# Optimization experiments

Hardware: AMD Instinct MI355X
Metric: run time of the kernel (lower is better)

## Reference

```python
import jax, jax.numpy as jnp
import numpy as np

NUM_NODES = 100000
EMBED_DIM = 128
HIDDEN = 128
NUM_EDGES = 1600000


def gcn_conv(x, W, b, src, dst, num_nodes):
    """PyG GCNConv: x' = D^{-1/2} (A+I) D^{-1/2} (x W) + b, symmetric norm with self-loops."""
    x = x @ W  # [N, out]
    loops = jnp.arange(num_nodes, dtype=src.dtype)
    s = jnp.concatenate([src, loops])  # sources incl. self-loops
    d = jnp.concatenate([dst, loops])  # targets incl. self-loops
    deg = jax.ops.segment_sum(jnp.ones_like(d, dtype=x.dtype), d, num_segments=num_nodes)
    dis = jnp.where(deg > 0, jax.lax.rsqrt(deg), 0.0)  # deg^{-1/2}, 0 where isolated
    norm = dis[s] * dis[d]  # [E+N]
    msg = x[s] * norm[:, None]  # gather + scale
    out = jax.ops.segment_sum(msg, d, num_segments=num_nodes)  # scatter-add
    return out + b


def setup_inputs() -> dict:
    key = jax.random.key(0)
    k1, k2, k3, k4, k5, k6 = jax.random.split(key, 6)
    edge_index = jax.random.randint(k1, (2, NUM_EDGES), 0, NUM_NODES, dtype=jnp.int64)
    edge_attr = jax.random.normal(k2, (NUM_EDGES,), dtype=jnp.float32)
    emb = jax.random.normal(k3, (NUM_NODES, EMBED_DIM), dtype=jnp.float32) * 0.1
    W1 = jax.random.normal(k4, (EMBED_DIM, HIDDEN), dtype=jnp.float32) * (1.0 / np.sqrt(EMBED_DIM))
    b1 = jnp.zeros((HIDDEN,), dtype=jnp.float32)
    W2 = jax.random.normal(k5, (HIDDEN, HIDDEN), dtype=jnp.float32) * (1.0 / np.sqrt(HIDDEN))
    b2 = jnp.zeros((HIDDEN,), dtype=jnp.float32)
    return {"edge_index": edge_index, "edge_attr": edge_attr, "emb": emb,
            "W1": W1, "b1": b1, "W2": W2, "b2": b2}


def reference(edge_index, edge_attr, emb, W1, b1, W2, b2):
    src, dst = edge_index[0], edge_index[1]
    x = gcn_conv(emb, W1, b1, src, dst, NUM_NODES)
    x = jax.nn.relu(x)
    x = gcn_conv(x, W2, b2, src, dst, NUM_NODES)
    return x
```

## Files before the change

### kernel.cpp

```cpp
#include <hip/hip_runtime.h>

#define EMB 128
#define NBUC 1024
#define NPART 256

typedef __attribute__((ext_vector_type(8))) short short8;
typedef __attribute__((ext_vector_type(4))) float f32x4;

__device__ __forceinline__ unsigned short f2bf(float f) {
    union { float f; unsigned int i; } v; v.f = f;
    unsigned int x = v.i;
    x += 0x7fffu + ((x >> 16) & 1u);
    return (unsigned short)(x >> 16);
}
__device__ __forceinline__ void acc_bf4(uint2 v, float& a0, float& a1, float& a2, float& a3) {
    union { unsigned int i; float f; } t;
    t.i = v.x << 16;          a0 += t.f;
    t.i = v.x & 0xffff0000u;  a1 += t.f;
    t.i = v.y << 16;          a2 += t.f;
    t.i = v.y & 0xffff0000u;  a3 += t.f;
}


__global__ __launch_bounds__(256) void p1_hist(const int* __restrict__ dst,
                                               int* __restrict__ BH, int E, int chunk) {
    __shared__ int h[NBUC];
    for (int i = threadIdx.x; i < NBUC; i += 256) h[i] = 0;
    __syncthreads();
    int s = blockIdx.x * chunk;
    int e = min(E, s + chunk);
    for (int i = s + threadIdx.x; i < e; i += 256)
        atomicAdd(&h[dst[i] >> 7], 1);
    __syncthreads();
    for (int i = threadIdx.x; i < NBUC; i += 256)
        BH[blockIdx.x * NBUC + i] = h[i];
}

__global__ __launch_bounds__(256) void p_tot(const int* __restrict__ BH,
                                             int* __restrict__ tot) {
    int b = blockIdx.x * 256 + threadIdx.x;
    int s = 0;
    for (int blk = 0; blk < NPART; ++blk) s += BH[blk * NBUC + b];
    tot[b] = s;
}

__global__ __launch_bounds__(1024) void p_scan(const int* __restrict__ tot,
                                               int* __restrict__ base, int E) {
    __shared__ int a[NBUC];
    int t = threadIdx.x;
    int v0 = tot[t];
    a[t] = v0;
    __syncthreads();
    for (int off = 1; off < NBUC; off <<= 1) {
        int v = (t >= off) ? a[t - off] : 0;
        __syncthreads();
        a[t] += v;
        __syncthreads();
    }
    base[t] = a[t] - v0;
    if (t == NBUC - 1) base[NBUC] = E;
}

__global__ __launch_bounds__(256) void p_offs(int* __restrict__ BH,
                                              const int* __restrict__ base) {
    int b = blockIdx.x * 256 + threadIdx.x;
    int run = base[b];
    for (int blk = 0; blk < NPART; ++blk) {
        int* p = &BH[blk * NBUC + b];
        int v = *p;
        *p = run;
        run += v;
    }
}

__global__ __launch_bounds__(256) void p2_scatter(const int* __restrict__ src,
                                                  const int* __restrict__ dst,
                                                  const int* __restrict__ BH,
                                                  int* __restrict__ part,
                                                  int E, int chunk) {
    __shared__ int cnt[NBUC];
    for (int i = threadIdx.x; i < NBUC; i += 256)
        cnt[i] = BH[blockIdx.x * NBUC + i];
    __syncthreads();
    int s = blockIdx.x * chunk;
    int e = min(E, s + chunk);
    for (int i = s + threadIdx.x; i < e; i += 256) {
        int d = dst[i];
        int pos = atomicAdd(&cnt[d >> 7], 1);
        part[pos] = src[i] | ((d & 127) << 17);
    }
}

__global__ __launch_bounds__(256) void p3_csr(const int* __restrict__ part,
                                              const int* __restrict__ base,
                                              int* __restrict__ R, int* __restrict__ adj,
                                              float* __restrict__ dis, int N, int E) {
    __shared__ int hist[128];
    __shared__ int sc[128];
    __shared__ int cnt[128];
    int b = blockIdx.x;
    int n0 = b * 128;
    int nn = min(128, N - n0);
    int s = base[b], e = base[b + 1];
    int t = threadIdx.x;

    if (t < 128) hist[t] = 0;
    __syncthreads();
    for (int i = s + t; i < e; i += 256)
        atomicAdd(&hist[part[i] >> 17], 1);
    __syncthreads();

    if (t < 128) sc[t] = hist[t];
    __syncthreads();
    for (int off = 1; off < 128; off <<= 1) {
        int v = 0;
        if (t < 128 && t >= off) v = sc[t - off];
        __syncthreads();
        if (t < 128) sc[t] += v;
        __syncthreads();
    }
    if (t < 128) {
        int excl = sc[t] - hist[t];
        cnt[t] = excl;
        if (t < nn) {
            R[n0 + t] = s + excl;
            dis[n0 + t] = rsqrtf((float)hist[t] + 1.0f);
        }
    }
    if (b == 0 && t == 0) R[N] = E;
    __syncthreads();

    for (int i = s + t; i < e; i += 256) {
        int p = part[i];
        int pos = atomicAdd(&cnt[p >> 17], 1);
        adj[s + pos] = p & 0x1FFFF;
    }
}

__global__ __launch_bounds__(256) void k_prep_w(const float* __restrict__ W,
                                                unsigned short* __restrict__ Ws) {
    int idx = blockIdx.x * 256 + threadIdx.x;
    int k = idx >> 7, n = idx & 127;
    int kk = k >> 5, q = (k >> 3) & 3, j = k & 7;
    int ct = n >> 4, nn = n & 15;
    int didx = ((((kk * 8 + ct) * 4 + q) * 16 + nn) << 3) + j;
    Ws[didx] = f2bf(W[idx]);
}

template <bool XBF16>
__global__ __launch_bounds__(256) void k_gemm_mfma(
    const void* Xv, const unsigned short* __restrict__ Wsw,
    const float* __restrict__ dis, unsigned short* Y, int N)
{
    __shared__ __align__(16) unsigned short lds[16384];

    {
        const uint4* srcp = (const uint4*)Wsw;
        uint4* dstp = (uint4*)lds;
        for (int i = threadIdx.x; i < 2048; i += 256) dstp[i] = srcp[i];
    }
    __syncthreads();

    const int wave = threadIdx.x >> 6;
    const int lane = threadIdx.x & 63;
    const int q = lane >> 4, nn = lane & 15;
    const int row0 = blockIdx.x * 64 + wave * 16;
    const int arow = row0 + nn;
    const int arc = arow < N ? arow : N - 1;

    f32x4 acc[8];
#pragma unroll
    for (int ct = 0; ct < 8; ++ct) acc[ct] = (f32x4){0.f, 0.f, 0.f, 0.f};

#pragma unroll
    for (int kk = 0; kk < 4; ++kk) {
        short8 af;
        if (XBF16) {
            af = *(const short8*)((const unsigned short*)Xv + (size_t)arc * EMB + kk * 32 + q * 8);
        } else {
            const float* xp = (const float*)Xv + (size_t)arc * EMB + kk * 32 + q * 8;
            float4 u0 = *(const float4*)xp;
            float4 u1 = *(const float4*)(xp + 4);
            af[0] = (short)f2bf(u0.x); af[1] = (short)f2bf(u0.y);
            af[2] = (short)f2bf(u0.z); af[3] = (short)f2bf(u0.w);
            af[4] = (short)f2bf(u1.x); af[5] = (short)f2bf(u1.y);
            af[6] = (short)f2bf(u1.z); af[7] = (short)f2bf(u1.w);
        }
#pragma unroll
        for (int ct = 0; ct < 8; ++ct) {
            short8 bf = ((const short8*)lds)[(kk * 8 + ct) * 64 + lane];
            acc[ct] = __builtin_amdgcn_mfma_f32_16x16x32_bf16(af, bf, acc[ct], 0, 0, 0);
        }
    }

    __syncthreads();

    float dv[4];
#pragma unroll
    for (int r = 0; r < 4; ++r) {
        int gm = row0 + q * 4 + r;
        dv[r] = dis[gm < N ? gm : N - 1];
    }
#pragma unroll
    for (int ct = 0; ct < 8; ++ct) {
#pragma unroll
        for (int r = 0; r < 4; ++r) {
            int ml = wave * 16 + q * 4 + r;
            lds[ml * 136 + ct * 16 + nn] = f2bf(acc[ct][r] * dv[r]);
        }
    }
    __syncthreads();

    const int rbase = blockIdx.x * 64;
    for (int i = threadIdx.x; i < 1024; i += 256) {
        int row = i >> 4, off = i & 15;
        int grow = rbase + row;
        if (grow < N) {
            uint4 v = *(const uint4*)(lds + row * 136 + off * 8);
            *((uint4*)(Y + (size_t)grow * EMB) + off) = v;
        }
    }
}

template <bool RELU, bool BF16OUT>
__global__ __launch_bounds__(256) void k_gather_finalize(
    const int* __restrict__ R, const int* __restrict__ adj,
    const unsigned short* __restrict__ Y, const float* __restrict__ dis,
    const float* __restrict__ bias, void* __restrict__ Outv, int N)
{
    int t = blockIdx.x * 256 + threadIdx.x;
    int n = t >> 5;
    if (n >= N) return;
    int j = (t & 31) * 4;

    int rs = R[n], re = R[n + 1];

    float a0 = 0.f, a1 = 0.f, a2 = 0.f, a3 = 0.f;
    uint2 sv = *(const uint2*)(Y + (size_t)n * EMB + j);
    acc_bf4(sv, a0, a1, a2, a3);

    int e = rs;
    for (; e + 3 < re; e += 4) {
        int s0 = adj[e], s1 = adj[e + 1], s2 = adj[e + 2], s3 = adj[e + 3];
        uint2 v0 = *(const uint2*)(Y + (size_t)s0 * EMB + j);
        uint2 v1 = *(const uint2*)(Y + (size_t)s1 * EMB + j);
        uint2 v2 = *(const uint2*)(Y + (size_t)s2 * EMB + j);
        uint2 v3 = *(const uint2*)(Y + (size_t)s3 * EMB + j);
        acc_bf4(v0, a0, a1, a2, a3);
        acc_bf4(v1, a0, a1, a2, a3);
        acc_bf4(v2, a0, a1, a2, a3);
        acc_bf4(v3, a0, a1, a2, a3);
    }
    for (; e < re; ++e) {
        uint2 v0 = *(const uint2*)(Y + (size_t)adj[e] * EMB + j);
        acc_bf4(v0, a0, a1, a2, a3);
    }

    float dv = dis[n];
    float4 b = *(const float4*)(bias + j);
    float o0 = dv * a0 + b.x;
    float o1 = dv * a1 + b.y;
    float o2 = dv * a2 + b.z;
    float o3 = dv * a3 + b.w;
    if (RELU) {
        o0 = fmaxf(o0, 0.f); o1 = fmaxf(o1, 0.f);
        o2 = fmaxf(o2, 0.f); o3 = fmaxf(o3, 0.f);
    }
    if (BF16OUT) {
        ushort4 o = { f2bf(o0), f2bf(o1), f2bf(o2), f2bf(o3) };
        *(ushort4*)((unsigned short*)Outv + (size_t)n * EMB + j) = o;
    } else {
        float4 o = { o0, o1, o2, o3 };
        *(float4*)((float*)Outv + (size_t)n * EMB + j) = o;
    }
}

extern "C" void kernel_launch(void* const* d_in, const int* in_sizes, int n_in,
                              void* d_out, int out_size, void* d_ws, size_t ws_size,
                              hipStream_t stream) {
    const int* ei = (const int*)d_in[0];
    const int E = in_sizes[0] / 2;
    const float* emb = (const float*)d_in[2];
    const int N = in_sizes[2] / EMB;
    const float* W1 = (const float*)d_in[3];
    const float* b1 = (const float*)d_in[4];
    const float* W2 = (const float*)d_in[5];
    const float* b2 = (const float*)d_in[6];
    float* out = (float*)d_out;

    const int* src = ei;
    const int* dstp = ei + E;

    char* w = (char*)d_ws;
    auto take = [&](size_t bytes) { char* p = w; w += (bytes + 511) & ~(size_t)511; return p; };
    float* dis  = (float*)take((size_t)N * 4);
    int*   R    = (int*)  take((size_t)(N + 1) * 4);
    int*   base = (int*)  take((size_t)(NBUC + 1) * 4);
    int*   tot  = (int*)  take((size_t)NBUC * 4);
    int*   adj  = (int*)  take((size_t)E * 4);
    unsigned short* W1s = (unsigned short*)take((size_t)EMB * EMB * 2);
    unsigned short* W2s = (unsigned short*)take((size_t)EMB * EMB * 2);
    unsigned short* Hb  = (unsigned short*)take((size_t)N * EMB * 2);
    int*   part = (int*)Hb;
    int*   BH   = (int*)((char*)Hb + (((size_t)E * 4 + 511) & ~(size_t)511));
    unsigned short* Y1b = (unsigned short*)d_out;

    const int NB = (N + 127) / 128;
    const int chunk = (E + NPART - 1) / NPART;
    const int gM = (N + 63) / 64;
    const int gG = (N * 32 + 255) / 256;

    p1_hist   <<<NPART, 256, 0, stream>>>(dstp, BH, E, chunk);
    p_tot     <<<NBUC / 256, 256, 0, stream>>>(BH, tot);
    p_scan    <<<1, NBUC, 0, stream>>>(tot, base, E);
    p_offs    <<<NBUC / 256, 256, 0, stream>>>(BH, base);
    p2_scatter<<<NPART, 256, 0, stream>>>(src, dstp, BH, part, E, chunk);
    p3_csr    <<<NB, 256, 0, stream>>>(part, base, R, adj, dis, N, E);

    k_prep_w<<<64, 256, 0, stream>>>(W1, W1s);
    k_prep_w<<<64, 256, 0, stream>>>(W2, W2s);

    k_gemm_mfma<false><<<gM, 256, 0, stream>>>(emb, W1s, dis, Y1b, N);
    k_gather_finalize<true, true><<<gG, 256, 0, stream>>>(R, adj, Y1b, dis, b1, Hb, N);

    k_gemm_mfma<true><<<gM, 256, 0, stream>>>(Hb, W2s, dis, Hb, N);
    k_gather_finalize<false, false><<<gG, 256, 0, stream>>>(R, adj, Hb, dis, b2, out, N);
}
```

Baseline: 343.8 us.

## Store bf16 activations slot-blocked so each XCD gathers one L2-resident feature slice

Rewrites the GEMM output and gather input into a feature-sliced layout: eight 16-column slots, each stored contiguously over all nodes. The gather kernel assigns slot = blockIdx & 7. Because blocks are dispatched round-robin across the 8 XCDs, each XCD then works on a single ~3.2MB slice, which can stay in its own L2 instead of spilling random gathers to HBM or Infinity Cache. The cost is that each edge index is now read eight times, and each neighbour access is a 32-byte read per lane pair rather than part of a 256-byte row read.

```diff
diff --git a/kernel.cpp b/kernel.cpp
--- a/kernel.cpp
+++ b/kernel.cpp
@@ -3,6 +3,7 @@
 #define EMB 128
 #define NBUC 1024
 #define NPART 256
+#define NSLOT 8
 
 typedef __attribute__((ext_vector_type(8))) short short8;
 typedef __attribute__((ext_vector_type(4))) float f32x4;
@@ -13,12 +14,16 @@
     x += 0x7fffu + ((x >> 16) & 1u);
     return (unsigned short)(x >> 16);
 }
-__device__ __forceinline__ void acc_bf4(uint2 v, float& a0, float& a1, float& a2, float& a3) {
+__device__ __forceinline__ void acc_bf8(uint4 v, float a[8]) {
     union { unsigned int i; float f; } t;
-    t.i = v.x << 16;          a0 += t.f;
-    t.i = v.x & 0xffff0000u;  a1 += t.f;
-    t.i = v.y << 16;          a2 += t.f;
-    t.i = v.y & 0xffff0000u;  a3 += t.f;
+    t.i = v.x << 16;          a[0] += t.f;
+    t.i = v.x & 0xffff0000u;  a[1] += t.f;
+    t.i = v.y << 16;          a[2] += t.f;
+    t.i = v.y & 0xffff0000u;  a[3] += t.f;
+    t.i = v.z << 16;          a[4] += t.f;
+    t.i = v.z & 0xffff0000u;  a[5] += t.f;
+    t.i = v.w << 16;          a[6] += t.f;
+    t.i = v.w & 0xffff0000u;  a[7] += t.f;
 }
 
 
@@ -176,7 +181,10 @@
     for (int kk = 0; kk < 4; ++kk) {
         short8 af;
         if (XBF16) {
-            af = *(const short8*)((const unsigned short*)Xv + (size_t)arc * EMB + kk * 32 + q * 8);
+            const int slot = kk * 2 + (q >> 1);
+            const int off = (q & 1) * 8;
+            af = *(const short8*)((const unsigned short*)Xv +
+                                  ((size_t)slot * N + arc) * 16 + off);
         } else {
             const float* xp = (const float*)Xv + (size_t)arc * EMB + kk * 32 + q * 8;
             float4 u0 = *(const float4*)xp;
@@ -213,65 +221,76 @@
 
     const int rbase = blockIdx.x * 64;
     for (int i = threadIdx.x; i < 1024; i += 256) {
-        int row = i >> 4, off = i & 15;
-        int grow = rbase + row;
+        int slot = i >> 7, r2 = (i >> 1) & 63, off = (i & 1) * 8;
+        int grow = rbase + r2;
         if (grow < N) {
-            uint4 v = *(const uint4*)(lds + row * 136 + off * 8);
-            *((uint4*)(Y + (size_t)grow * EMB) + off) = v;
+            uint4 v = *(const uint4*)(lds + r2 * 136 + slot * 16 + off);
+            *(uint4*)(Y + ((size_t)slot * N + grow) * 16 + off) = v;
         }
     }
 }
 
 template <bool RELU, bool BF16OUT>
-__global__ __launch_bounds__(256) void k_gather_finalize(
+__global__ __launch_bounds__(256) void k_gather_blocked(
     const int* __restrict__ R, const int* __restrict__ adj,
-    const unsigned short* __restrict__ Y, const float* __restrict__ dis,
+    const unsigned short* __restrict__ Yb, const float* __restrict__ dis,
     const float* __restrict__ bias, void* __restrict__ Outv, int N)
 {
-    int t = blockIdx.x * 256 + threadIdx.x;
-    int n = t >> 5;
+    const int slot = blockIdx.x & 7;
+    const int n = (blockIdx.x >> 3) * 128 + (threadIdx.x >> 1);
+    const int h = threadIdx.x & 1;
     if (n >= N) return;
-    int j = (t & 31) * 4;
+
+    const unsigned short* __restrict__ Ys = Yb + (size_t)slot * N * 16 + h * 8;
+
+    float a[8];
+#pragma unroll
+    for (int k = 0; k < 8; ++k) a[k] = 0.f;
+
+    uint4 sv = *(const uint4*)(Ys + (size_t)n * 16);
+    acc_bf8(sv, a);
 
     int rs = R[n], re = R[n + 1];
-
-    float a0 = 0.f, a1 = 0.f, a2 = 0.f, a3 = 0.f;
-    uint2 sv = *(const uint2*)(Y + (size_t)n * EMB + j);
-    acc_bf4(sv, a0, a1, a2, a3);
-
     int e = rs;
-    for (; e + 3 < re; e += 4) {
+    for (; e + 4 <= re; e += 4) {
         int s0 = adj[e], s1 = adj[e + 1], s2 = adj[e + 2], s3 = adj[e + 3];
-        uint2 v0 = *(const uint2*)(Y + (size_t)s0 * EMB + j);
-        uint2 v1 = *(const uint2*)(Y + (size_t)s1 * EMB + j);
-        uint2 v2 = *(const uint2*)(Y + (size_t)s2 * EMB + j);
-        uint2 v3 = *(const uint2*)(Y + (size_t)s3 * EMB + j);
-        acc_bf4(v0, a0, a1, a2, a3);
-        acc_bf4(v1, a0, a1, a2, a3);
-        acc_bf4(v2, a0, a1, a2, a3);
-        acc_bf4(v3, a0, a1, a2, a3);
+        uint4 v0 = *(const uint4*)(Ys + (size_t)s0 * 16);
+        uint4 v1 = *(const uint4*)(Ys + (size_t)s1 * 16);
+        uint4 v2 = *(const uint4*)(Ys + (size_t)s2 * 16);
+        uint4 v3 = *(const uint4*)(Ys + (size_t)s3 * 16);
+        acc_bf8(v0, a); acc_bf8(v1, a); acc_bf8(v2, a); acc_bf8(v3, a);
     }
     for (; e < re; ++e) {
-        uint2 v0 = *(const uint2*)(Y + (size_t)adj[e] * EMB + j);
-        acc_bf4(v0, a0, a1, a2, a3);
-    }
-
-    float dv = dis[n];
-    float4 b = *(const float4*)(bias + j);
-    float o0 = dv * a0 + b.x;
-    float o1 = dv * a1 + b.y;
-    float o2 = dv * a2 + b.z;
-    float o3 = dv * a3 + b.w;
+        uint4 v = *(const uint4*)(Ys + (size_t)adj[e] * 16);
+        acc_bf8(v, a);
+    }
+
+    const float dv = dis[n];
+    const int dbase = slot * 16 + h * 8;
+    float4 b0 = *(const float4*)(bias + dbase);
+    float4 b1 = *(const float4*)(bias + dbase + 4);
+    float o[8];
+    o[0] = dv * a[0] + b0.x; o[1] = dv * a[1] + b0.y;
+    o[2] = dv * a[2] + b0.z; o[3] = dv * a[3] + b0.w;
+    o[4] = dv * a[4] + b1.x; o[5] = dv * a[5] + b1.y;
+    o[6] = dv * a[6] + b1.z; o[7] = dv * a[7] + b1.w;
     if (RELU) {
-        o0 = fmaxf(o0, 0.f); o1 = fmaxf(o1, 0.f);
-        o2 = fmaxf(o2, 0.f); o3 = fmaxf(o3, 0.f);
+#pragma unroll
+        for (int k = 0; k < 8; ++k) o[k] = fmaxf(o[k], 0.f);
     }
     if (BF16OUT) {
-        ushort4 o = { f2bf(o0), f2bf(o1), f2bf(o2), f2bf(o3) };
-        *(ushort4*)((unsigned short*)Outv + (size_t)n * EMB + j) = o;
+        uint4 pk;
+        pk.x = (unsigned)f2bf(o[0]) | ((unsigned)f2bf(o[1]) << 16);
+        pk.y = (unsigned)f2bf(o[2]) | ((unsigned)f2bf(o[3]) << 16);
+        pk.z = (unsigned)f2bf(o[4]) | ((unsigned)f2bf(o[5]) << 16);
+        pk.w = (unsigned)f2bf(o[6]) | ((unsigned)f2bf(o[7]) << 16);
+        *(uint4*)((unsigned short*)Outv + ((size_t)slot * N + n) * 16 + h * 8) = pk;
     } else {
-        float4 o = { o0, o1, o2, o3 };
-        *(float4*)((float*)Outv + (size_t)n * EMB + j) = o;
+        float* op = (float*)Outv + (size_t)n * EMB + dbase;
+        float4 q0 = { o[0], o[1], o[2], o[3] };
+        float4 q1 = { o[4], o[5], o[6], o[7] };
+        *(float4*)op = q0;
+        *(float4*)(op + 4) = q1;
     }
 }
 
@@ -308,7 +327,7 @@
     const int NB = (N + 127) / 128;
     const int chunk = (E + NPART - 1) / NPART;
     const int gM = (N + 63) / 64;
-    const int gG = (N * 32 + 255) / 256;
+    const int gG = NB * NSLOT;
 
     p1_hist   <<<NPART, 256, 0, stream>>>(dstp, BH, E, chunk);
     p_tot     <<<NBUC / 256, 256, 0, stream>>>(BH, tot);
@@ -321,8 +340,8 @@
     k_prep_w<<<64, 256, 0, stream>>>(W2, W2s);
 
     k_gemm_mfma<false><<<gM, 256, 0, stream>>>(emb, W1s, dis, Y1b, N);
-    k_gather_finalize<true, true><<<gG, 256, 0, stream>>>(R, adj, Y1b, dis, b1, Hb, N);
+    k_gather_blocked<true, true><<<gG, 256, 0, stream>>>(R, adj, Y1b, dis, b1, Hb, N);
 
     k_gemm_mfma<true><<<gM, 256, 0, stream>>>(Hb, W2s, dis, Hb, N);
-    k_gather_finalize<false, false><<<gG, 256, 0, stream>>>(R, adj, Hb, dis, b2, out, N);
-}
+    k_gather_blocked<false, false><<<gG, 256, 0, stream>>>(R, adj, Hb, dis, b2, out, N);
+}
```

Result: slower. 398.9 us (+16.0%).
